# Kernel tuning notes

Measured on AMD Instinct MI355X. Metric: run time of the kernel, lower is better.

The kernel has to match this reference:

```python
import jax, jax.numpy as jnp
import numpy as np

N_VERTS = 200_000
EMBD_D = 256
M_QUERIES = 500_000


def setup_inputs() -> dict:
    key = jax.random.key(0)
    ks = jax.random.split(key, 8)
    s = 1.0 / np.sqrt(EMBD_D)
    return {
        "p_vertices": jax.random.randint(ks[0], (M_QUERIES,), 0, N_VERTS, dtype=jnp.int64)
        if jax.config.jax_enable_x64 else jax.random.randint(ks[0], (M_QUERIES,), 0, N_VERTS, dtype=jnp.int32),
        "q_vertices": jax.random.randint(ks[1], (M_QUERIES,), 0, N_VERTS, dtype=jnp.int32),
        "embedding": jax.random.normal(ks[2], (N_VERTS, EMBD_D), dtype=jnp.float32),
        "w1": jax.random.normal(ks[3], (EMBD_D, EMBD_D), dtype=jnp.float32) * s,
        "b1": jnp.zeros((EMBD_D,), jnp.float32),
        "w2": jax.random.normal(ks[4], (EMBD_D, EMBD_D), dtype=jnp.float32) * s,
        "b2": jnp.zeros((EMBD_D,), jnp.float32),
        "w3": jax.random.normal(ks[5], (EMBD_D, 1), dtype=jnp.float32) * s,
        "b3": jnp.zeros((1,), jnp.float32),
    }


def reference(p_vertices, q_vertices, embedding, w1, b1, w2, b2, w3, b3):
    # gather two rows per query and take elementwise squared difference  [M, D]
    embd = (embedding[p_vertices] - embedding[q_vertices]) ** 2
    # small MLP decoder: 256 -> 256 -> 256 -> 1, ReLU activations
    h = jax.nn.relu(embd @ w1 + b1)
    h = jax.nn.relu(h @ w2 + b2)
    pred = (h @ w3 + b3).squeeze(-1)  # [M]
    return pred
```

## Files before the change

kernel.cpp:

```cpp
#include <hip/hip_runtime.h>
#include <hip/hip_bf16.h>
#include <stdint.h>


#define D 256
#define MT 64
#define THREADS 256

typedef __attribute__((ext_vector_type(8))) short short8;
typedef __attribute__((ext_vector_type(4))) float f32x4;

__device__ __forceinline__ unsigned short f2bf(float f) {
    unsigned int u = __float_as_uint(f);
    unsigned int r = (u + 0x7FFFu + ((u >> 16) & 1u)) >> 16;
    return (unsigned short)r;
}
__device__ __forceinline__ float bflo(unsigned int u) { return __uint_as_float(u << 16); }
__device__ __forceinline__ float bfhi(unsigned int u) { return __uint_as_float(u & 0xFFFF0000u); }

__device__ __forceinline__ unsigned int sqdiff2(unsigned int p, unsigned int q) {
    float d0 = bflo(p) - bflo(q);
    float d1 = bfhi(p) - bfhi(q);
    return (unsigned int)f2bf(d0 * d0) | ((unsigned int)f2bf(d1 * d1) << 16);
}

__global__ void pack_w_kernel(const float* __restrict__ w1,
                              const float* __restrict__ w2,
                              unsigned short* __restrict__ out) {
    int tid = blockIdx.x * blockDim.x + threadIdx.x;
    int mat = tid >> 13;
    const float* W = mat ? w2 : w1;
    unsigned short* o = out + mat * 65536;
    int rem  = tid & 8191;
    int nt   = rem >> 9;
    int ks   = (rem >> 6) & 7;
    int lane = rem & 63;
    int kbase = ks * 32 + (lane >> 4) * 8;
    int n     = nt * 16 + (lane & 15);
    short8 v;
#pragma unroll
    for (int j = 0; j < 8; ++j)
        v[j] = (short)f2bf(W[(kbase + j) * 256 + n]);
    *reinterpret_cast<short8*>(o + (((nt * 8) + ks) * 64 + lane) * 8) = v;
}

template <bool BF16T>
__launch_bounds__(THREADS, 3)
__global__ void fused_kernel(const int* __restrict__ pv,
                             const int* __restrict__ qv,
                             const float* __restrict__ embf,
                             const unsigned short* __restrict__ embb,
                             const float* __restrict__ b1,
                             const float* __restrict__ b2,
                             const float* __restrict__ w3,
                             const float* __restrict__ b3,
                             const unsigned short* __restrict__ wpack,
                             float* __restrict__ out,
                             int M) {
    __shared__ unsigned char lds_a[MT * 512];
    __shared__ float lds_part[4][MT];

    const int tid  = threadIdx.x;
    const int lane = tid & 63;
    const int wave = tid >> 6;
    const int base = blockIdx.x * MT;

    if (BF16T) {
#pragma unroll
        for (int it = 0; it < 8; ++it) {
            int r  = wave * 16 + it * 2 + (lane >> 5);
            int gi = base + r;
            int pi = 0, qi = 0;
            if (gi < M) { pi = pv[gi]; qi = qv[gi]; }
            int c = lane & 31;
            uint4 a = *(reinterpret_cast<const uint4*>(embb + (size_t)pi * D) + c);
            uint4 b = *(reinterpret_cast<const uint4*>(embb + (size_t)qi * D) + c);
            uint4 o;
            o.x = sqdiff2(a.x, b.x);
            o.y = sqdiff2(a.y, b.y);
            o.z = sqdiff2(a.z, b.z);
            o.w = sqdiff2(a.w, b.w);
            unsigned int unit = (unsigned int)c ^ (unsigned int)(r & 31);
            *reinterpret_cast<uint4*>(&lds_a[(unsigned int)r * 512u + (unit << 4)]) = o;
        }
    } else {
#pragma unroll
        for (int rr = 0; rr < 16; ++rr) {
            int r  = wave * 16 + rr;
            int gi = base + r;
            int pi = 0, qi = 0;
            if (gi < M) { pi = pv[gi]; qi = qv[gi]; }
            const float4* ep = reinterpret_cast<const float4*>(embf + (size_t)pi * D);
            const float4* eq = reinterpret_cast<const float4*>(embf + (size_t)qi * D);
            float4 a = ep[lane];
            float4 b = eq[lane];
            float d0 = a.x - b.x, d1 = a.y - b.y, d2 = a.z - b.z, d3 = a.w - b.w;
            unsigned int lo = (unsigned int)f2bf(d0 * d0) | ((unsigned int)f2bf(d1 * d1) << 16);
            unsigned int hi = (unsigned int)f2bf(d2 * d2) | ((unsigned int)f2bf(d3 * d3) << 16);
            unsigned int unit = (unsigned int)(lane >> 1) ^ (unsigned int)(r & 31);
            unsigned int addr = (unsigned int)r * 512u + (unit << 4) + (unsigned int)(lane & 1) * 8u;
            *reinterpret_cast<uint2*>(&lds_a[addr]) = make_uint2(lo, hi);
        }
    }
    __syncthreads();

    const int wn    = wave;
    const int nbase = wn * 64;
    const int l15   = lane & 15;
    const int quad  = lane >> 4;

    const short8* wp1 = reinterpret_cast<const short8*>(wpack);
    const short8* wp2 = reinterpret_cast<const short8*>(wpack + 65536);

    f32x4 acc[4][4];
    short8 bb0[4], bb1[4];

#define LOADB(buf, wp, ksv)                                            \
    _Pragma("unroll")                                                  \
    for (int ct = 0; ct < 4; ++ct)                                     \
        buf[ct] = (wp)[((((nbase >> 4) + ct) * 8) + (ksv)) * 64 + lane];

#define LOADA(af, ksv)                                                               \
    _Pragma("unroll")                                                                \
    for (int mt = 0; mt < 4; ++mt) {                                                 \
        int r = mt * 16 + l15;                                                       \
        unsigned int unit = (unsigned int)((ksv) * 4 + quad) ^ (unsigned int)(r & 31);\
        af[mt] = *reinterpret_cast<const short8*>(                                   \
            &lds_a[(unsigned int)r * 512u + (unit << 4)]);                           \
    }

#define MFMA16(bu)                                                      \
    _Pragma("unroll")                                                   \
    for (int mt = 0; mt < 4; ++mt)                                      \
        _Pragma("unroll")                                               \
        for (int ct = 0; ct < 4; ++ct)                                  \
            acc[mt][ct] = __builtin_amdgcn_mfma_f32_16x16x32_bf16(      \
                af[mt], bu[ct], acc[mt][ct], 0, 0, 0);

#pragma unroll
    for (int mt = 0; mt < 4; ++mt)
#pragma unroll
        for (int ct = 0; ct < 4; ++ct)
            acc[mt][ct] = (f32x4){0.f, 0.f, 0.f, 0.f};

    LOADB(bb0, wp1, 0)
    LOADB(bb1, wp1, 1)
#pragma unroll
    for (int ks = 0; ks < 8; ++ks) {
        short8 af[4];
        LOADA(af, ks)
        if (ks & 1) {
            MFMA16(bb1)
            if (ks + 2 < 8) LOADB(bb1, wp1, ks + 2)
        } else {
            MFMA16(bb0)
            if (ks + 2 < 8) LOADB(bb0, wp1, ks + 2)
        }
    }

    __syncthreads();

#pragma unroll
    for (int ct = 0; ct < 4; ++ct) {
        int c = nbase + ct * 16 + l15;
        float bias = b1[c];
#pragma unroll
        for (int mt = 0; mt < 4; ++mt) {
#pragma unroll
            for (int j = 0; j < 4; ++j) {
                float v = acc[mt][ct][j] + bias;
                v = fmaxf(v, 0.f);
                int r = mt * 16 + quad * 4 + j;
                unsigned int unit = (unsigned int)(c >> 3) ^ (unsigned int)(r & 31);
                unsigned int addr = (unsigned int)r * 512u + (unit << 4) + (unsigned int)(c & 7) * 2u;
                *reinterpret_cast<unsigned short*>(&lds_a[addr]) = f2bf(v);
            }
        }
    }
    __syncthreads();

#pragma unroll
    for (int mt = 0; mt < 4; ++mt)
#pragma unroll
        for (int ct = 0; ct < 4; ++ct)
            acc[mt][ct] = (f32x4){0.f, 0.f, 0.f, 0.f};

    LOADB(bb0, wp2, 0)
    LOADB(bb1, wp2, 1)
#pragma unroll
    for (int ks = 0; ks < 8; ++ks) {
        short8 af[4];
        LOADA(af, ks)
        if (ks & 1) {
            MFMA16(bb1)
            if (ks + 2 < 8) LOADB(bb1, wp2, ks + 2)
        } else {
            MFMA16(bb0)
            if (ks + 2 < 8) LOADB(bb0, wp2, ks + 2)
        }
    }

    float part[4][4];
#pragma unroll
    for (int mt = 0; mt < 4; ++mt)
#pragma unroll
        for (int j = 0; j < 4; ++j)
            part[mt][j] = 0.f;

#pragma unroll
    for (int ct = 0; ct < 4; ++ct) {
        int c = nbase + ct * 16 + l15;
        float bias = b2[c];
        float w3v  = w3[c];
#pragma unroll
        for (int mt = 0; mt < 4; ++mt)
#pragma unroll
            for (int j = 0; j < 4; ++j) {
                float v = acc[mt][ct][j] + bias;
                v = fmaxf(v, 0.f);
                part[mt][j] += v * w3v;
            }
    }

#pragma unroll
    for (int msk = 8; msk >= 1; msk >>= 1)
#pragma unroll
        for (int mt = 0; mt < 4; ++mt)
#pragma unroll
            for (int j = 0; j < 4; ++j)
                part[mt][j] += __shfl_xor(part[mt][j], msk, 64);

    if (l15 == 0) {
#pragma unroll
        for (int mt = 0; mt < 4; ++mt)
#pragma unroll
            for (int j = 0; j < 4; ++j) {
                int r = mt * 16 + quad * 4 + j;
                lds_part[wn][r] = part[mt][j];
            }
    }
    __syncthreads();

    if (tid < MT) {
        int gi = base + tid;
        if (gi < M) {
            float s = lds_part[0][tid] + lds_part[1][tid] +
                      lds_part[2][tid] + lds_part[3][tid] + b3[0];
            out[gi] = s;
        }
    }
}

extern "C" void kernel_launch(void* const* d_in, const int* in_sizes, int n_in,
                              void* d_out, int out_size, void* d_ws, size_t ws_size,
                              hipStream_t stream) {
    const int*   pv  = (const int*)d_in[0];
    const int*   qv  = (const int*)d_in[1];
    const float* emb = (const float*)d_in[2];
    const float* w1  = (const float*)d_in[3];
    const float* b1  = (const float*)d_in[4];
    const float* w2  = (const float*)d_in[5];
    const float* b2  = (const float*)d_in[6];
    const float* w3  = (const float*)d_in[7];
    const float* b3  = (const float*)d_in[8];
    float* out = (float*)d_out;
    const int M  = in_sizes[0];

    unsigned short* wpack = (unsigned short*)d_ws;

    pack_w_kernel<<<32, 512, 0, stream>>>(w1, w2, wpack);

    int nblk = (M + MT - 1) / MT;
    fused_kernel<false><<<nblk, THREADS, 0, stream>>>(
        pv, qv, emb, nullptr, b1, b2, w3, b3, wpack, out, M);
}
```

Baseline: 548.1 us.

## Make fused MLP kernel persistent with double-buffered gather prefetch

Turns the fused gather+MLP kernel into a persistent kernel of at most 512 blocks that loop over 64-row tiles. The embedding gathers for the next tile are issued into registers while the current tile's MFMA GEMMs run, then written into a second LDS buffer. This is meant to hide random-gather memory latency behind compute. It also raises MFMA wave priority with s_setprio and drops occupancy to 2 blocks per SIMD, which adds register pressure (prefetched float4s stay live across the GEMMs) and may leave fewer blocks in flight than the hardware can hold.

Result: slower. 1.560 ms (+184.7%).

```diff
diff --git a/kernel.cpp b/kernel.cpp
--- a/kernel.cpp
+++ b/kernel.cpp
@@ -6,6 +6,7 @@
 #define D 256
 #define MT 64
 #define THREADS 256
+#define PERSIST_BLOCKS 512
 
 typedef __attribute__((ext_vector_type(8))) short short8;
 typedef __attribute__((ext_vector_type(4))) float f32x4;
@@ -14,14 +15,6 @@
     unsigned int u = __float_as_uint(f);
     unsigned int r = (u + 0x7FFFu + ((u >> 16) & 1u)) >> 16;
     return (unsigned short)r;
-}
-__device__ __forceinline__ float bflo(unsigned int u) { return __uint_as_float(u << 16); }
-__device__ __forceinline__ float bfhi(unsigned int u) { return __uint_as_float(u & 0xFFFF0000u); }
-
-__device__ __forceinline__ unsigned int sqdiff2(unsigned int p, unsigned int q) {
-    float d0 = bflo(p) - bflo(q);
-    float d1 = bfhi(p) - bfhi(q);
-    return (unsigned int)f2bf(d0 * d0) | ((unsigned int)f2bf(d1 * d1) << 16);
 }
 
 __global__ void pack_w_kernel(const float* __restrict__ w1,
@@ -44,12 +37,10 @@
     *reinterpret_cast<short8*>(o + (((nt * 8) + ks) * 64 + lane) * 8) = v;
 }
 
-template <bool BF16T>
-__launch_bounds__(THREADS, 3)
+__launch_bounds__(THREADS, 2)
 __global__ void fused_kernel(const int* __restrict__ pv,
                              const int* __restrict__ qv,
                              const float* __restrict__ embf,
-                             const unsigned short* __restrict__ embb,
                              const float* __restrict__ b1,
                              const float* __restrict__ b2,
                              const float* __restrict__ w3,
@@ -57,52 +48,16 @@
                              const unsigned short* __restrict__ wpack,
                              float* __restrict__ out,
                              int M) {
-    __shared__ unsigned char lds_a[MT * 512];
+    __shared__ unsigned char lds_a[2][MT * 512];
     __shared__ float lds_part[4][MT];
 
     const int tid  = threadIdx.x;
     const int lane = tid & 63;
     const int wave = tid >> 6;
-    const int base = blockIdx.x * MT;
-
-    if (BF16T) {
-#pragma unroll
-        for (int it = 0; it < 8; ++it) {
-            int r  = wave * 16 + it * 2 + (lane >> 5);
-            int gi = base + r;
-            int pi = 0, qi = 0;
-            if (gi < M) { pi = pv[gi]; qi = qv[gi]; }
-            int c = lane & 31;
-            uint4 a = *(reinterpret_cast<const uint4*>(embb + (size_t)pi * D) + c);
-            uint4 b = *(reinterpret_cast<const uint4*>(embb + (size_t)qi * D) + c);
-            uint4 o;
-            o.x = sqdiff2(a.x, b.x);
-            o.y = sqdiff2(a.y, b.y);
-            o.z = sqdiff2(a.z, b.z);
-            o.w = sqdiff2(a.w, b.w);
-            unsigned int unit = (unsigned int)c ^ (unsigned int)(r & 31);
-            *reinterpret_cast<uint4*>(&lds_a[(unsigned int)r * 512u + (unit << 4)]) = o;
-        }
-    } else {
-#pragma unroll
-        for (int rr = 0; rr < 16; ++rr) {
-            int r  = wave * 16 + rr;
-            int gi = base + r;
-            int pi = 0, qi = 0;
-            if (gi < M) { pi = pv[gi]; qi = qv[gi]; }
-            const float4* ep = reinterpret_cast<const float4*>(embf + (size_t)pi * D);
-            const float4* eq = reinterpret_cast<const float4*>(embf + (size_t)qi * D);
-            float4 a = ep[lane];
-            float4 b = eq[lane];
-            float d0 = a.x - b.x, d1 = a.y - b.y, d2 = a.z - b.z, d3 = a.w - b.w;
-            unsigned int lo = (unsigned int)f2bf(d0 * d0) | ((unsigned int)f2bf(d1 * d1) << 16);
-            unsigned int hi = (unsigned int)f2bf(d2 * d2) | ((unsigned int)f2bf(d3 * d3) << 16);
-            unsigned int unit = (unsigned int)(lane >> 1) ^ (unsigned int)(r & 31);
-            unsigned int addr = (unsigned int)r * 512u + (unit << 4) + (unsigned int)(lane & 1) * 8u;
-            *reinterpret_cast<uint2*>(&lds_a[addr]) = make_uint2(lo, hi);
-        }
-    }
-    __syncthreads();
+    const int ntiles = (M + MT - 1) / MT;
+
+    int t = blockIdx.x;
+    if (t >= ntiles) return;
 
     const int wn    = wave;
     const int nbase = wn * 64;
@@ -112,21 +67,48 @@
     const short8* wp1 = reinterpret_cast<const short8*>(wpack);
     const short8* wp2 = reinterpret_cast<const short8*>(wpack + 65536);
 
-    f32x4 acc[4][4];
-    short8 bb0[4], bb1[4];
+    float4 pf[8], qf[8];
+
+#define ISSUE(tb_, h_)                                                       \
+    _Pragma("unroll")                                                        \
+    for (int rr = 0; rr < 8; ++rr) {                                         \
+        int r  = wave * 16 + (h_) * 8 + rr;                                  \
+        int gi = (tb_) + r;                                                  \
+        int pi = 0, qi = 0;                                                  \
+        if (gi < M) { pi = pv[gi]; qi = qv[gi]; }                            \
+        pf[rr] = reinterpret_cast<const float4*>(embf + (size_t)pi * D)[lane]; \
+        qf[rr] = reinterpret_cast<const float4*>(embf + (size_t)qi * D)[lane]; \
+    }
+
+#define PROCESS(h_, buf_)                                                    \
+    _Pragma("unroll")                                                        \
+    for (int rr = 0; rr < 8; ++rr) {                                         \
+        int r = wave * 16 + (h_) * 8 + rr;                                   \
+        float4 a = pf[rr], b = qf[rr];                                       \
+        float d0 = a.x - b.x, d1 = a.y - b.y;                                \
+        float d2 = a.z - b.z, d3 = a.w - b.w;                                \
+        unsigned int lo = (unsigned int)f2bf(d0 * d0) |                      \
+                          ((unsigned int)f2bf(d1 * d1) << 16);               \
+        unsigned int hi = (unsigned int)f2bf(d2 * d2) |                      \
+                          ((unsigned int)f2bf(d3 * d3) << 16);               \
+        unsigned int unit = (unsigned int)(lane >> 1) ^ (unsigned int)(r & 31);\
+        unsigned int addr = (unsigned int)r * 512u + (unit << 4) +           \
+                            (unsigned int)(lane & 1) * 8u;                   \
+        *reinterpret_cast<uint2*>(&(buf_)[addr]) = make_uint2(lo, hi);       \
+    }
 
 #define LOADB(buf, wp, ksv)                                            \
     _Pragma("unroll")                                                  \
     for (int ct = 0; ct < 4; ++ct)                                     \
         buf[ct] = (wp)[((((nbase >> 4) + ct) * 8) + (ksv)) * 64 + lane];
 
-#define LOADA(af, ksv)                                                               \
+#define LOADA(af, ab_, ksv)                                                          \
     _Pragma("unroll")                                                                \
     for (int mt = 0; mt < 4; ++mt) {                                                 \
         int r = mt * 16 + l15;                                                       \
         unsigned int unit = (unsigned int)((ksv) * 4 + quad) ^ (unsigned int)(r & 31);\
         af[mt] = *reinterpret_cast<const short8*>(                                   \
-            &lds_a[(unsigned int)r * 512u + (unit << 4)]);                           \
+            &(ab_)[(unsigned int)r * 512u + (unit << 4)]);                           \
     }
 
 #define MFMA16(bu)                                                      \
@@ -137,117 +119,155 @@
             acc[mt][ct] = __builtin_amdgcn_mfma_f32_16x16x32_bf16(      \
                 af[mt], bu[ct], acc[mt][ct], 0, 0, 0);
 
-#pragma unroll
-    for (int mt = 0; mt < 4; ++mt)
-#pragma unroll
-        for (int ct = 0; ct < 4; ++ct)
-            acc[mt][ct] = (f32x4){0.f, 0.f, 0.f, 0.f};
-
-    LOADB(bb0, wp1, 0)
-    LOADB(bb1, wp1, 1)
-#pragma unroll
-    for (int ks = 0; ks < 8; ++ks) {
-        short8 af[4];
-        LOADA(af, ks)
-        if (ks & 1) {
-            MFMA16(bb1)
-            if (ks + 2 < 8) LOADB(bb1, wp1, ks + 2)
-        } else {
-            MFMA16(bb0)
-            if (ks + 2 < 8) LOADB(bb0, wp1, ks + 2)
-        }
-    }
-
+    f32x4 acc[4][4];
+    short8 bb0[4], bb1[4];
+
+    {
+        unsigned char* nb = lds_a[0];
+        ISSUE(t * MT, 0)
+        PROCESS(0, nb)
+        ISSUE(t * MT, 1)
+        PROCESS(1, nb)
+    }
     __syncthreads();
 
-#pragma unroll
-    for (int ct = 0; ct < 4; ++ct) {
-        int c = nbase + ct * 16 + l15;
-        float bias = b1[c];
-#pragma unroll
-        for (int mt = 0; mt < 4; ++mt) {
-#pragma unroll
-            for (int j = 0; j < 4; ++j) {
-                float v = acc[mt][ct][j] + bias;
-                v = fmaxf(v, 0.f);
-                int r = mt * 16 + quad * 4 + j;
-                unsigned int unit = (unsigned int)(c >> 3) ^ (unsigned int)(r & 31);
-                unsigned int addr = (unsigned int)r * 512u + (unit << 4) + (unsigned int)(c & 7) * 2u;
-                *reinterpret_cast<unsigned short*>(&lds_a[addr]) = f2bf(v);
-            }
-        }
-    }
-    __syncthreads();
-
-#pragma unroll
-    for (int mt = 0; mt < 4; ++mt)
-#pragma unroll
-        for (int ct = 0; ct < 4; ++ct)
-            acc[mt][ct] = (f32x4){0.f, 0.f, 0.f, 0.f};
-
-    LOADB(bb0, wp2, 0)
-    LOADB(bb1, wp2, 1)
-#pragma unroll
-    for (int ks = 0; ks < 8; ++ks) {
-        short8 af[4];
-        LOADA(af, ks)
-        if (ks & 1) {
-            MFMA16(bb1)
-            if (ks + 2 < 8) LOADB(bb1, wp2, ks + 2)
-        } else {
-            MFMA16(bb0)
-            if (ks + 2 < 8) LOADB(bb0, wp2, ks + 2)
-        }
-    }
-
-    float part[4][4];
-#pragma unroll
-    for (int mt = 0; mt < 4; ++mt)
-#pragma unroll
-        for (int j = 0; j < 4; ++j)
-            part[mt][j] = 0.f;
-
-#pragma unroll
-    for (int ct = 0; ct < 4; ++ct) {
-        int c = nbase + ct * 16 + l15;
-        float bias = b2[c];
-        float w3v  = w3[c];
+    int cur = 0;
+    for (; t < ntiles; t += gridDim.x) {
+        const int tb   = t * MT;
+        const int tnb  = (t + (int)gridDim.x) * MT;
+        const bool pre = (t + (int)gridDim.x) < ntiles;
+        unsigned char* ab = lds_a[cur];
+        unsigned char* nb = lds_a[cur ^ 1];
+
+        if (pre) ISSUE(tnb, 0)
+
 #pragma unroll
         for (int mt = 0; mt < 4; ++mt)
 #pragma unroll
-            for (int j = 0; j < 4; ++j) {
-                float v = acc[mt][ct][j] + bias;
-                v = fmaxf(v, 0.f);
-                part[mt][j] += v * w3v;
-            }
-    }
-
-#pragma unroll
-    for (int msk = 8; msk >= 1; msk >>= 1)
+            for (int ct = 0; ct < 4; ++ct)
+                acc[mt][ct] = (f32x4){0.f, 0.f, 0.f, 0.f};
+
+        LOADB(bb0, wp1, 0)
+        LOADB(bb1, wp1, 1)
+#pragma unroll
+        for (int ks = 0; ks < 8; ++ks) {
+            short8 af[4];
+            LOADA(af, ab, ks)
+            __builtin_amdgcn_s_setprio(1);
+            if (ks & 1) {
+                MFMA16(bb1)
+                __builtin_amdgcn_s_setprio(0);
+                if (ks + 2 < 8) LOADB(bb1, wp1, ks + 2)
+            } else {
+                MFMA16(bb0)
+                __builtin_amdgcn_s_setprio(0);
+                if (ks + 2 < 8) LOADB(bb0, wp1, ks + 2)
+            }
+        }
+
+        __syncthreads();
+
+#pragma unroll
+        for (int ct = 0; ct < 4; ++ct) {
+            int c = nbase + ct * 16 + l15;
+            float bias = b1[c];
+#pragma unroll
+            for (int mt = 0; mt < 4; ++mt) {
+#pragma unroll
+                for (int j = 0; j < 4; ++j) {
+                    float v = acc[mt][ct][j] + bias;
+                    v = fmaxf(v, 0.f);
+                    int r = mt * 16 + quad * 4 + j;
+                    unsigned int unit = (unsigned int)(c >> 3) ^ (unsigned int)(r & 31);
+                    unsigned int addr = (unsigned int)r * 512u + (unit << 4) + (unsigned int)(c & 7) * 2u;
+                    *reinterpret_cast<unsigned short*>(&ab[addr]) = f2bf(v);
+                }
+            }
+        }
+
+        if (pre) {
+            PROCESS(0, nb)
+            ISSUE(tnb, 1)
+        }
+        __syncthreads();
+
 #pragma unroll
         for (int mt = 0; mt < 4; ++mt)
 #pragma unroll
+            for (int ct = 0; ct < 4; ++ct)
+                acc[mt][ct] = (f32x4){0.f, 0.f, 0.f, 0.f};
+
+        LOADB(bb0, wp2, 0)
+        LOADB(bb1, wp2, 1)
+#pragma unroll
+        for (int ks = 0; ks < 8; ++ks) {
+            short8 af[4];
+            LOADA(af, ab, ks)
+            __builtin_amdgcn_s_setprio(1);
+            if (ks & 1) {
+                MFMA16(bb1)
+                __builtin_amdgcn_s_setprio(0);
+                if (ks + 2 < 8) LOADB(bb1, wp2, ks + 2)
+            } else {
+                MFMA16(bb0)
+                __builtin_amdgcn_s_setprio(0);
+                if (ks + 2 < 8) LOADB(bb0, wp2, ks + 2)
+            }
+        }
+
+        float part[4][4];
+#pragma unroll
+        for (int mt = 0; mt < 4; ++mt)
+#pragma unroll
             for (int j = 0; j < 4; ++j)
-                part[mt][j] += __shfl_xor(part[mt][j], msk, 64);
-
-    if (l15 == 0) {
-#pragma unroll
-        for (int mt = 0; mt < 4; ++mt)
-#pragma unroll
-            for (int j = 0; j < 4; ++j) {
-                int r = mt * 16 + quad * 4 + j;
-                lds_part[wn][r] = part[mt][j];
-            }
-    }
-    __syncthreads();
-
-    if (tid < MT) {
-        int gi = base + tid;
-        if (gi < M) {
-            float s = lds_part[0][tid] + lds_part[1][tid] +
-                      lds_part[2][tid] + lds_part[3][tid] + b3[0];
-            out[gi] = s;
-        }
+                part[mt][j] = 0.f;
+
+#pragma unroll
+        for (int ct = 0; ct < 4; ++ct) {
+            int c = nbase + ct * 16 + l15;
+            float bias = b2[c];
+            float w3v  = w3[c];
+#pragma unroll
+            for (int mt = 0; mt < 4; ++mt)
+#pragma unroll
+                for (int j = 0; j < 4; ++j) {
+                    float v = acc[mt][ct][j] + bias;
+                    v = fmaxf(v, 0.f);
+                    part[mt][j] += v * w3v;
+                }
+        }
+
+#pragma unroll
+        for (int msk = 8; msk >= 1; msk >>= 1)
+#pragma unroll
+            for (int mt = 0; mt < 4; ++mt)
+#pragma unroll
+                for (int j = 0; j < 4; ++j)
+                    part[mt][j] += __shfl_xor(part[mt][j], msk, 64);
+
+        if (l15 == 0) {
+#pragma unroll
+            for (int mt = 0; mt < 4; ++mt)
+#pragma unroll
+                for (int j = 0; j < 4; ++j) {
+                    int r = mt * 16 + quad * 4 + j;
+                    lds_part[wn][r] = part[mt][j];
+                }
+        }
+        __syncthreads();
+
+        if (tid < MT) {
+            int gi = tb + tid;
+            if (gi < M) {
+                float s = lds_part[0][tid] + lds_part[1][tid] +
+                          lds_part[2][tid] + lds_part[3][tid] + b3[0];
+                out[gi] = s;
+            }
+        }
+
+        if (pre) PROCESS(1, nb)
+        __syncthreads();
+        cur ^= 1;
     }
 }
 
@@ -270,7 +290,8 @@
 
     pack_w_kernel<<<32, 512, 0, stream>>>(w1, w2, wpack);
 
-    int nblk = (M + MT - 1) / MT;
-    fused_kernel<false><<<nblk, THREADS, 0, stream>>>(
-        pv, qv, emb, nullptr, b1, b2, w3, b3, wpack, out, M);
-}
+    int ntiles = (M + MT - 1) / MT;
+    int nblk = ntiles < PERSIST_BLOCKS ? ntiles : PERSIST_BLOCKS;
+    fused_kernel<<<nblk, THREADS, 0, stream>>>(
+        pv, qv, emb, b1, b2, w3, b3, wpack, out, M);
+}
```
